# Kernel tuning notes

Measured on AMD Instinct MI355X. Metric: run time of the kernel, lower is better.

The kernel has to match this reference:

```python
import jax, jax.numpy as jnp
import numpy as np

S, N, H, E, V, K = 128, 256, 1024, 512, 32000, 1024  # seq, batch, hidden, embed, vocab, energy channels


def setup_inputs() -> dict:
    key = jax.random.key(0)
    ks = jax.random.split(key, 10)
    s = 0.02
    return {
        "input": jax.random.randint(ks[0], (N,), 0, V),
        "encoder_states": jax.random.normal(ks[1], (S, N, H), jnp.float32),
        "hidden": jax.random.normal(ks[2], (1, N, H), jnp.float32),
        "cell": jax.random.normal(ks[3], (1, N, H), jnp.float32),
        "emb": jax.random.normal(ks[4], (V, E), jnp.float32) * s,
        "W_energy": jax.random.normal(ks[5], (K, 2 * H), jnp.float32) * s,
        "b_energy": jnp.zeros((K,), jnp.float32),
        "W_ih": jax.random.normal(ks[6], (4 * H, H + E), jnp.float32) * s,
        "b_ih": jnp.zeros((4 * H,), jnp.float32),
        "W_hh": jax.random.normal(ks[7], (4 * H, H), jnp.float32) * s,
        "b_hh": jnp.zeros((4 * H,), jnp.float32),
        "W_fc": jax.random.normal(ks[8], (V, H), jnp.float32) * s,
        "b_fc": jnp.zeros((V,), jnp.float32),
    }


def reference(input, encoder_states, hidden, cell, emb, W_energy, b_energy,
              W_ih, b_ih, W_hh, b_hh, W_fc, b_fc):
    seq = encoder_states.shape[0]
    n = encoder_states.shape[1]
    h0 = hidden[0]                                   # [N,H]
    c0 = cell[0]                                     # [N,H]
    emb_x = emb[input]                               # [N,E]

    # additive-attention energy: cat(hidden repeated over S, encoder_states) -> Linear -> ReLU
    h_rep = jnp.broadcast_to(hidden, (seq, n, hidden.shape[2]))
    cat = jnp.concatenate([h_rep, encoder_states], axis=2)          # [S,N,2H]
    energy = jax.nn.relu(jnp.einsum('snh,kh->snk', cat, W_energy) + b_energy)  # [S,N,K]
    # softmax over dim 0 (sequence), independently per (n,k) channel
    attn_last = jax.nn.softmax(energy[..., -1], axis=0)             # [S,N]
    # einsum('snk,snl->knl')[-1] only uses channel k=K-1; contract just that slice
    ctx = jnp.einsum('sn,snl->nl', attn_last, encoder_states)       # [N,H]

    # single-step LSTM (PyTorch gate order i,f,g,o)
    rnn_in = jnp.concatenate([ctx, emb_x], axis=1)                  # [N,H+E]
    gates = rnn_in @ W_ih.T + b_ih + h0 @ W_hh.T + b_hh             # [N,4H]
    i, f, g, o = jnp.split(gates, 4, axis=1)
    c1 = jax.nn.sigmoid(f) * c0 + jax.nn.sigmoid(i) * jnp.tanh(g)
    h1 = jax.nn.sigmoid(o) * jnp.tanh(c1)

    predictions = h1 @ W_fc.T + b_fc                                # [N,V]
    return predictions, h1[None], c1[None]
```

## Files before the change

kernel.cpp:

```cpp
#include <hip/hip_runtime.h>

#define S_DIM 128
#define N_DIM 256
#define H_DIM 1024
#define E_DIM 512
#define V_DIM 32000
#define KE_DIM 1024
#define CIN 2560
#define G4 4096

typedef unsigned short u16;
typedef __bf16 bf16x8 __attribute__((ext_vector_type(8)));
typedef float  f32x4  __attribute__((ext_vector_type(4)));

union U16x8 { uint4 u; bf16x8 b; };

__device__ __forceinline__ unsigned f2bf(float x) {
  unsigned u = __float_as_uint(x);
  return (u + 0x7FFFu + ((u >> 16) & 1u)) >> 16;
}
__device__ __forceinline__ unsigned pk2(float a, float b) {
  return f2bf(a) | (f2bf(b) << 16);
}

__device__ __forceinline__ bf16x8 frag_from_global(const u16* p) {
  U16x8 t; t.u = *(const uint4*)p; return t.b;
}
__device__ __forceinline__ bf16x8 frag_from_lds(const u16* base, int byteoff) {
  U16x8 t; t.u = *(const uint4*)((const char*)base + byteoff); return t.b;
}

__device__ __forceinline__ int loff64(int row, int k) {
  return row * 128 + ((((k >> 3) ^ (row & 7)) << 4) | ((k & 7) << 1));
}
__device__ __forceinline__ int loff128(int row, int k) {
  return row * 256 + ((((k >> 3) ^ (row & 7)) << 4) | ((k & 7) << 1));
}

__device__ __forceinline__ f32x4 mfma16(bf16x8 a, bf16x8 b, f32x4 c) {
  return __builtin_amdgcn_mfma_f32_16x16x32_bf16(a, b, c, 0, 0, 0);
}

__global__ __launch_bounds__(256) void k1_attn(
    const float* __restrict__ enc, const float* __restrict__ hid,
    const float* __restrict__ Wen, const float* __restrict__ ben,
    const int* __restrict__ inp, const float* __restrict__ emb,
    u16* __restrict__ A2)
{
  __shared__ float s_acc[4][H_DIM];
  __shared__ float s_ml[8];
  const int n = blockIdx.x;
  const int t = threadIdx.x;
  const int wave = t >> 6, lane = t & 63;

  const float* Wrow = Wen + (KE_DIM - 1) * (2 * H_DIM);
  float4 we[4];
  #pragma unroll
  for (int ks = 0; ks < 4; ++ks)
    we[ks] = *(const float4*)(Wrow + H_DIM + ks * 256 + lane * 4);

  float hd = 0.f;
  #pragma unroll
  for (int ks = 0; ks < 4; ++ks) {
    float4 wh = *(const float4*)(Wrow + ks * 256 + lane * 4);
    float4 hv = *(const float4*)(hid + n * H_DIM + ks * 256 + lane * 4);
    hd += wh.x * hv.x + wh.y * hv.y + wh.z * hv.z + wh.w * hv.w;
  }
  #pragma unroll
  for (int off = 32; off > 0; off >>= 1) hd += __shfl_xor(hd, off, 64);
  const float ebase = hd + ben[KE_DIM - 1];

  float m = -INFINITY, l = 0.f;
  float4 acc[4];
  #pragma unroll
  for (int ks = 0; ks < 4; ++ks) acc[ks] = make_float4(0.f, 0.f, 0.f, 0.f);

  const long rstride = 4L * N_DIM * H_DIM;
  const float* p = enc + ((long)wave * N_DIM + n) * H_DIM + lane * 4;
  float4 cur[4];
  #pragma unroll
  for (int ks = 0; ks < 4; ++ks) cur[ks] = *(const float4*)(p + ks * 256);

  for (int s = wave; s < S_DIM; s += 4) {
    float4 nxt[4];
    const float* pn = p + rstride;
    const bool has = (s + 4 < S_DIM);
    if (has) {
      #pragma unroll
      for (int ks = 0; ks < 4; ++ks) nxt[ks] = *(const float4*)(pn + ks * 256);
    }
    float d = 0.f;
    #pragma unroll
    for (int ks = 0; ks < 4; ++ks)
      d += we[ks].x * cur[ks].x + we[ks].y * cur[ks].y +
           we[ks].z * cur[ks].z + we[ks].w * cur[ks].w;
    #pragma unroll
    for (int off = 32; off > 0; off >>= 1) d += __shfl_xor(d, off, 64);
    const float e  = fmaxf(ebase + d, 0.f);
    const float nm = fmaxf(m, e);
    const float sc = __expf(m - nm);
    const float pe = __expf(e - nm);
    l = l * sc + pe;
    #pragma unroll
    for (int ks = 0; ks < 4; ++ks) {
      acc[ks].x = acc[ks].x * sc + pe * cur[ks].x;
      acc[ks].y = acc[ks].y * sc + pe * cur[ks].y;
      acc[ks].z = acc[ks].z * sc + pe * cur[ks].z;
      acc[ks].w = acc[ks].w * sc + pe * cur[ks].w;
    }
    m = nm;
    if (has) {
      #pragma unroll
      for (int ks = 0; ks < 4; ++ks) cur[ks] = nxt[ks];
    }
    p = pn;
  }

  #pragma unroll
  for (int ks = 0; ks < 4; ++ks)
    *(float4*)&s_acc[wave][ks * 256 + lane * 4] = acc[ks];
  if (lane == 0) { s_ml[wave] = m; s_ml[4 + wave] = l; }
  __syncthreads();

  const float M = fmaxf(fmaxf(s_ml[0], s_ml[1]), fmaxf(s_ml[2], s_ml[3]));
  const float f0 = __expf(s_ml[0] - M), f1 = __expf(s_ml[1] - M);
  const float f2 = __expf(s_ml[2] - M), f3 = __expf(s_ml[3] - M);
  const float L = s_ml[4] * f0 + s_ml[5] * f1 + s_ml[6] * f2 + s_ml[7] * f3;
  const float invL = 1.0f / L;
  {
    const int e0 = t * 4;
    float v0 = (s_acc[0][e0+0]*f0 + s_acc[1][e0+0]*f1 + s_acc[2][e0+0]*f2 + s_acc[3][e0+0]*f3) * invL;
    float v1 = (s_acc[0][e0+1]*f0 + s_acc[1][e0+1]*f1 + s_acc[2][e0+1]*f2 + s_acc[3][e0+1]*f3) * invL;
    float v2 = (s_acc[0][e0+2]*f0 + s_acc[1][e0+2]*f1 + s_acc[2][e0+2]*f2 + s_acc[3][e0+2]*f3) * invL;
    float v3 = (s_acc[0][e0+3]*f0 + s_acc[1][e0+3]*f1 + s_acc[2][e0+3]*f2 + s_acc[3][e0+3]*f3) * invL;
    uint2 pk; pk.x = pk2(v0, v1); pk.y = pk2(v2, v3);
    *(uint2*)&A2[(long)n * CIN + e0] = pk;
  }

  const int idx = inp[n];
  for (int j = t; j < E_DIM + H_DIM; j += 256) {
    float v = (j < E_DIM) ? emb[(long)idx * E_DIM + j]
                          : hid[n * H_DIM + (j - E_DIM)];
    A2[(long)n * CIN + H_DIM + j] = (u16)f2bf(v);
  }
}

__global__ __launch_bounds__(256) void k2_gates(
    const u16* __restrict__ A2, const float* __restrict__ Wih,
    const float* __restrict__ bih, const float* __restrict__ Whh,
    const float* __restrict__ bhh, float* __restrict__ gates)
{
  __shared__ u16 Blds[16 * 128];
  const int t = threadIdx.x;
  const int wave = t >> 6, lane = t & 63;
  const int quad = lane >> 4, l15 = lane & 15;
  const int j0 = blockIdx.x * 16;
  const int br = t >> 4;
  const int bk = (t & 15) * 8;

  f32x4 acc[4];
  #pragma unroll
  for (int mt = 0; mt < 4; ++mt) acc[mt] = (f32x4){0.f, 0.f, 0.f, 0.f};

  const float* s0 = Wih + (long)(j0 + br) * 1536 + bk;
  float4 v0 = *(const float4*)s0;
  float4 v1 = *(const float4*)(s0 + 4);

  for (int kt = 0; kt < 20; ++kt) {
    const int k0 = kt * 128;
    uint4 pk;
    pk.x = pk2(v0.x, v0.y); pk.y = pk2(v0.z, v0.w);
    pk.z = pk2(v1.x, v1.y); pk.w = pk2(v1.z, v1.w);
    *(uint4*)((char*)Blds + loff128(br, bk)) = pk;
    if (kt + 1 < 20) {
      const int kn = k0 + 128 + bk;
      const float* sn = (kn < 1536) ? (Wih + (long)(j0 + br) * 1536 + kn)
                                    : (Whh + (long)(j0 + br) * 1024 + (kn - 1536));
      v0 = *(const float4*)sn;
      v1 = *(const float4*)(sn + 4);
    }
    __syncthreads();
    #pragma unroll
    for (int kstep = 0; kstep < 4; ++kstep) {
      const int kl = kstep * 32 + quad * 8;
      const bf16x8 bfrag = frag_from_lds(Blds, loff128(l15, kl));
      #pragma unroll
      for (int mt = 0; mt < 4; ++mt) {
        const int row = wave * 64 + mt * 16 + l15;
        const bf16x8 afrag = frag_from_global(A2 + (long)row * CIN + k0 + kl);
        acc[mt] = mfma16(afrag, bfrag, acc[mt]);
      }
    }
    __syncthreads();
  }

  const float bias = bih[j0 + l15] + bhh[j0 + l15];
  #pragma unroll
  for (int mt = 0; mt < 4; ++mt) {
    #pragma unroll
    for (int r = 0; r < 4; ++r) {
      const int row = wave * 64 + mt * 16 + quad * 4 + r;
      gates[(long)row * G4 + j0 + l15] = acc[mt][r] + bias;
    }
  }
}

__global__ __launch_bounds__(256) void k2b_lstm(
    const float* __restrict__ gates, const float* __restrict__ cell,
    float* __restrict__ h1, float* __restrict__ c1, u16* __restrict__ h1b)
{
  const int i = blockIdx.x * 256 + threadIdx.x;
  const int n = i >> 10, h = i & 1023;
  const float* g = gates + (long)n * G4 + h;
  const float gi = g[0], gf = g[1024], gg = g[2048], go = g[3072];
  const float si = 1.f / (1.f + __expf(-gi));
  const float sf = 1.f / (1.f + __expf(-gf));
  const float so = 1.f / (1.f + __expf(-go));
  const float tg = tanhf(gg);
  const float cv = sf * cell[i] + si * tg;
  const float hv = so * tanhf(cv);
  c1[i] = cv;
  h1[i] = hv;
  h1b[i] = (u16)f2bf(hv);
}

__global__ __launch_bounds__(256) void k3_fc(
    const u16* __restrict__ h1b, const float* __restrict__ Wfc,
    const float* __restrict__ bfc, float* __restrict__ out)
{
  __shared__ u16 Blds[64 * 64];
  const int t = threadIdx.x;
  const int wave = t >> 6, lane = t & 63;
  const int quad = lane >> 4, l15 = lane & 15;
  const int j0 = blockIdx.x * 64;
  const int br = t >> 2;
  const int bk = (t & 3) * 16;
  const float* bsrc = Wfc + (long)(j0 + br) * 1024 + bk;

  f32x4 acc[4][4];
  #pragma unroll
  for (int mt = 0; mt < 4; ++mt)
    #pragma unroll
    for (int nt = 0; nt < 4; ++nt) acc[mt][nt] = (f32x4){0.f, 0.f, 0.f, 0.f};

  float4 v0 = *(const float4*)(bsrc);
  float4 v1 = *(const float4*)(bsrc + 4);
  float4 v2 = *(const float4*)(bsrc + 8);
  float4 v3 = *(const float4*)(bsrc + 12);

  for (int kt = 0; kt < 16; ++kt) {
    const int k0 = kt * 64;
    uint4 pa, pb;
    pa.x = pk2(v0.x, v0.y); pa.y = pk2(v0.z, v0.w);
    pa.z = pk2(v1.x, v1.y); pa.w = pk2(v1.z, v1.w);
    pb.x = pk2(v2.x, v2.y); pb.y = pk2(v2.z, v2.w);
    pb.z = pk2(v3.x, v3.y); pb.w = pk2(v3.z, v3.w);
    *(uint4*)((char*)Blds + loff64(br, bk)) = pa;
    *(uint4*)((char*)Blds + loff64(br, bk + 8)) = pb;
    if (kt + 1 < 16) {
      const float* sn = bsrc + (k0 + 64);
      v0 = *(const float4*)(sn);
      v1 = *(const float4*)(sn + 4);
      v2 = *(const float4*)(sn + 8);
      v3 = *(const float4*)(sn + 12);
    }
    __syncthreads();
    #pragma unroll
    for (int kstep = 0; kstep < 2; ++kstep) {
      const int kl = kstep * 32 + quad * 8;
      bf16x8 bfrag[4], afrag[4];
      #pragma unroll
      for (int nt = 0; nt < 4; ++nt)
        bfrag[nt] = frag_from_lds(Blds, loff64(nt * 16 + l15, kl));
      #pragma unroll
      for (int mt = 0; mt < 4; ++mt)
        afrag[mt] = frag_from_global(h1b + (long)(wave * 64 + mt * 16 + l15) * 1024 + k0 + kl);
      #pragma unroll
      for (int mt = 0; mt < 4; ++mt)
        #pragma unroll
        for (int nt = 0; nt < 4; ++nt)
          acc[mt][nt] = mfma16(afrag[mt], bfrag[nt], acc[mt][nt]);
    }
    __syncthreads();
  }

  #pragma unroll
  for (int nt = 0; nt < 4; ++nt) {
    const float bv = bfc[j0 + nt * 16 + l15];
    #pragma unroll
    for (int mt = 0; mt < 4; ++mt) {
      #pragma unroll
      for (int r = 0; r < 4; ++r) {
        const int row = wave * 64 + mt * 16 + quad * 4 + r;
        out[(long)row * V_DIM + j0 + nt * 16 + l15] = acc[mt][nt][r] + bv;
      }
    }
  }
}

extern "C" void kernel_launch(void* const* d_in, const int* in_sizes, int n_in,
                              void* d_out, int out_size, void* d_ws, size_t ws_size,
                              hipStream_t stream) {
  const int*   inp  = (const int*)  d_in[0];
  const float* enc  = (const float*)d_in[1];
  const float* hid  = (const float*)d_in[2];
  const float* cell = (const float*)d_in[3];
  const float* emb  = (const float*)d_in[4];
  const float* Wen  = (const float*)d_in[5];
  const float* ben  = (const float*)d_in[6];
  const float* Wih  = (const float*)d_in[7];
  const float* bih  = (const float*)d_in[8];
  const float* Whh  = (const float*)d_in[9];
  const float* bhh  = (const float*)d_in[10];
  const float* Wfc  = (const float*)d_in[11];
  const float* bfc  = (const float*)d_in[12];

  float* out  = (float*)d_out;
  float* pred = out;
  float* h1   = out + (long)N_DIM * V_DIM;
  float* c1   = h1 + (long)N_DIM * H_DIM;

  char* ws = (char*)d_ws;
  u16*   A2    = (u16*)ws;
  float* gates = (float*)(ws + 1310720);
  u16*   h1b   = (u16*)(ws + 1310720 + 4194304);

  k1_attn <<<N_DIM,            256, 0, stream>>>(enc, hid, Wen, ben, inp, emb, A2);
  k2_gates<<<G4 / 16,          256, 0, stream>>>(A2, Wih, bih, Whh, bhh, gates);
  k2b_lstm<<<(N_DIM*H_DIM)/256,256, 0, stream>>>(gates, cell, h1, c1, h1b);
  k3_fc   <<<V_DIM / 64,       256, 0, stream>>>(h1b, Wfc, bfc, pred);
}
```

Baseline: 425.8 us.

## Fuse attention, LSTM gates and FC into one cooperative persistent kernel

Replaces the four kernel launches with a single cooperative kernel of 256 blocks of 512 threads, using grid.sync between the attention, gate and FC phases. The gate GEMM is reorganised so each block computes the i/f/g/o columns for 4 hidden units and applies the LSTM cell in place, which removes the fp32 gates buffer and the separate elementwise kernel. The FC phase becomes a persistent loop over vocabulary tiles with smaller per-wave tiles. The intent is to remove launch gaps and gate-buffer traffic. The cost is only 256 blocks for the FC GEMM, so fewer waves are resident to hide memory latency, plus the overhead of the grid barriers.

```diff
diff --git a/kernel.cpp b/kernel.cpp
--- a/kernel.cpp
+++ b/kernel.cpp
@@ -1,4 +1,7 @@
 #include <hip/hip_runtime.h>
+#include <hip/hip_cooperative_groups.h>
+
+namespace cg = cooperative_groups;
 
 #define S_DIM 128
 #define N_DIM 256
@@ -7,7 +10,6 @@
 #define V_DIM 32000
 #define KE_DIM 1024
 #define CIN 2560
-#define G4 4096
 
 typedef unsigned short u16;
 typedef __bf16 bf16x8 __attribute__((ext_vector_type(8)));
@@ -41,258 +43,249 @@
   return __builtin_amdgcn_mfma_f32_16x16x32_bf16(a, b, c, 0, 0, 0);
 }
 
-__global__ __launch_bounds__(256) void k1_attn(
-    const float* __restrict__ enc, const float* __restrict__ hid,
-    const float* __restrict__ Wen, const float* __restrict__ ben,
-    const int* __restrict__ inp, const float* __restrict__ emb,
-    u16* __restrict__ A2)
+struct ShP1 { float acc[8][H_DIM]; float ml[16]; };
+struct ShP2 { u16 b[16 * 128]; float sg[256][17]; };
+struct ShP3 { u16 b[64 * 64]; };
+union ShAll { ShP1 p1; ShP2 p2; ShP3 p3; };
+
+__global__ __launch_bounds__(512) void kmega(
+    const int*   __restrict__ inp,  const float* __restrict__ enc,
+    const float* __restrict__ hid,  const float* __restrict__ cell0,
+    const float* __restrict__ emb,  const float* __restrict__ Wen,
+    const float* __restrict__ ben,  const float* __restrict__ Wih,
+    const float* __restrict__ bih,  const float* __restrict__ Whh,
+    const float* __restrict__ bhh,  const float* __restrict__ Wfc,
+    const float* __restrict__ bfc,
+    u16* __restrict__ A2, u16* __restrict__ h1b,
+    float* __restrict__ pred, float* __restrict__ h1, float* __restrict__ c1)
 {
-  __shared__ float s_acc[4][H_DIM];
-  __shared__ float s_ml[8];
-  const int n = blockIdx.x;
-  const int t = threadIdx.x;
-  const int wave = t >> 6, lane = t & 63;
-
-  const float* Wrow = Wen + (KE_DIM - 1) * (2 * H_DIM);
-  float4 we[4];
-  #pragma unroll
-  for (int ks = 0; ks < 4; ++ks)
-    we[ks] = *(const float4*)(Wrow + H_DIM + ks * 256 + lane * 4);
-
-  float hd = 0.f;
-  #pragma unroll
-  for (int ks = 0; ks < 4; ++ks) {
-    float4 wh = *(const float4*)(Wrow + ks * 256 + lane * 4);
-    float4 hv = *(const float4*)(hid + n * H_DIM + ks * 256 + lane * 4);
-    hd += wh.x * hv.x + wh.y * hv.y + wh.z * hv.z + wh.w * hv.w;
-  }
-  #pragma unroll
-  for (int off = 32; off > 0; off >>= 1) hd += __shfl_xor(hd, off, 64);
-  const float ebase = hd + ben[KE_DIM - 1];
-
-  float m = -INFINITY, l = 0.f;
-  float4 acc[4];
-  #pragma unroll
-  for (int ks = 0; ks < 4; ++ks) acc[ks] = make_float4(0.f, 0.f, 0.f, 0.f);
-
-  const long rstride = 4L * N_DIM * H_DIM;
-  const float* p = enc + ((long)wave * N_DIM + n) * H_DIM + lane * 4;
-  float4 cur[4];
-  #pragma unroll
-  for (int ks = 0; ks < 4; ++ks) cur[ks] = *(const float4*)(p + ks * 256);
-
-  for (int s = wave; s < S_DIM; s += 4) {
-    float4 nxt[4];
-    const float* pn = p + rstride;
-    const bool has = (s + 4 < S_DIM);
-    if (has) {
-      #pragma unroll
-      for (int ks = 0; ks < 4; ++ks) nxt[ks] = *(const float4*)(pn + ks * 256);
-    }
-    float d = 0.f;
-    #pragma unroll
-    for (int ks = 0; ks < 4; ++ks)
-      d += we[ks].x * cur[ks].x + we[ks].y * cur[ks].y +
-           we[ks].z * cur[ks].z + we[ks].w * cur[ks].w;
-    #pragma unroll
-    for (int off = 32; off > 0; off >>= 1) d += __shfl_xor(d, off, 64);
-    const float e  = fmaxf(ebase + d, 0.f);
-    const float nm = fmaxf(m, e);
-    const float sc = __expf(m - nm);
-    const float pe = __expf(e - nm);
-    l = l * sc + pe;
-    #pragma unroll
-    for (int ks = 0; ks < 4; ++ks) {
-      acc[ks].x = acc[ks].x * sc + pe * cur[ks].x;
-      acc[ks].y = acc[ks].y * sc + pe * cur[ks].y;
-      acc[ks].z = acc[ks].z * sc + pe * cur[ks].z;
-      acc[ks].w = acc[ks].w * sc + pe * cur[ks].w;
-    }
-    m = nm;
-    if (has) {
-      #pragma unroll
-      for (int ks = 0; ks < 4; ++ks) cur[ks] = nxt[ks];
-    }
-    p = pn;
-  }
-
-  #pragma unroll
-  for (int ks = 0; ks < 4; ++ks)
-    *(float4*)&s_acc[wave][ks * 256 + lane * 4] = acc[ks];
-  if (lane == 0) { s_ml[wave] = m; s_ml[4 + wave] = l; }
-  __syncthreads();
-
-  const float M = fmaxf(fmaxf(s_ml[0], s_ml[1]), fmaxf(s_ml[2], s_ml[3]));
-  const float f0 = __expf(s_ml[0] - M), f1 = __expf(s_ml[1] - M);
-  const float f2 = __expf(s_ml[2] - M), f3 = __expf(s_ml[3] - M);
-  const float L = s_ml[4] * f0 + s_ml[5] * f1 + s_ml[6] * f2 + s_ml[7] * f3;
-  const float invL = 1.0f / L;
-  {
-    const int e0 = t * 4;
-    float v0 = (s_acc[0][e0+0]*f0 + s_acc[1][e0+0]*f1 + s_acc[2][e0+0]*f2 + s_acc[3][e0+0]*f3) * invL;
-    float v1 = (s_acc[0][e0+1]*f0 + s_acc[1][e0+1]*f1 + s_acc[2][e0+1]*f2 + s_acc[3][e0+1]*f3) * invL;
-    float v2 = (s_acc[0][e0+2]*f0 + s_acc[1][e0+2]*f1 + s_acc[2][e0+2]*f2 + s_acc[3][e0+2]*f3) * invL;
-    float v3 = (s_acc[0][e0+3]*f0 + s_acc[1][e0+3]*f1 + s_acc[2][e0+3]*f2 + s_acc[3][e0+3]*f3) * invL;
-    uint2 pk; pk.x = pk2(v0, v1); pk.y = pk2(v2, v3);
-    *(uint2*)&A2[(long)n * CIN + e0] = pk;
-  }
-
-  const int idx = inp[n];
-  for (int j = t; j < E_DIM + H_DIM; j += 256) {
-    float v = (j < E_DIM) ? emb[(long)idx * E_DIM + j]
-                          : hid[n * H_DIM + (j - E_DIM)];
-    A2[(long)n * CIN + H_DIM + j] = (u16)f2bf(v);
-  }
-}
-
-__global__ __launch_bounds__(256) void k2_gates(
-    const u16* __restrict__ A2, const float* __restrict__ Wih,
-    const float* __restrict__ bih, const float* __restrict__ Whh,
-    const float* __restrict__ bhh, float* __restrict__ gates)
-{
-  __shared__ u16 Blds[16 * 128];
-  const int t = threadIdx.x;
+  __shared__ ShAll sh;
+  cg::grid_group grid = cg::this_grid();
+  const int t    = threadIdx.x;
   const int wave = t >> 6, lane = t & 63;
   const int quad = lane >> 4, l15 = lane & 15;
-  const int j0 = blockIdx.x * 16;
-  const int br = t >> 4;
-  const int bk = (t & 15) * 8;
-
-  f32x4 acc[4];
-  #pragma unroll
-  for (int mt = 0; mt < 4; ++mt) acc[mt] = (f32x4){0.f, 0.f, 0.f, 0.f};
-
-  const float* s0 = Wih + (long)(j0 + br) * 1536 + bk;
-  float4 v0 = *(const float4*)s0;
-  float4 v1 = *(const float4*)(s0 + 4);
-
-  for (int kt = 0; kt < 20; ++kt) {
-    const int k0 = kt * 128;
-    uint4 pk;
-    pk.x = pk2(v0.x, v0.y); pk.y = pk2(v0.z, v0.w);
-    pk.z = pk2(v1.x, v1.y); pk.w = pk2(v1.z, v1.w);
-    *(uint4*)((char*)Blds + loff128(br, bk)) = pk;
-    if (kt + 1 < 20) {
-      const int kn = k0 + 128 + bk;
-      const float* sn = (kn < 1536) ? (Wih + (long)(j0 + br) * 1536 + kn)
-                                    : (Whh + (long)(j0 + br) * 1024 + (kn - 1536));
-      v0 = *(const float4*)sn;
-      v1 = *(const float4*)(sn + 4);
-    }
+
+  {
+    const int n = blockIdx.x;
+    const float* Wrow = Wen + (KE_DIM - 1) * (2 * H_DIM);
+    float4 we[4];
+    #pragma unroll
+    for (int ks = 0; ks < 4; ++ks)
+      we[ks] = *(const float4*)(Wrow + H_DIM + ks * 256 + lane * 4);
+
+    float hd = 0.f;
+    #pragma unroll
+    for (int ks = 0; ks < 4; ++ks) {
+      float4 wh = *(const float4*)(Wrow + ks * 256 + lane * 4);
+      float4 hv = *(const float4*)(hid + n * H_DIM + ks * 256 + lane * 4);
+      hd += wh.x * hv.x + wh.y * hv.y + wh.z * hv.z + wh.w * hv.w;
+    }
+    #pragma unroll
+    for (int off = 32; off > 0; off >>= 1) hd += __shfl_xor(hd, off, 64);
+    const float ebase = hd + ben[KE_DIM - 1];
+
+    float m = -INFINITY, l = 0.f;
+    float4 acc[4];
+    #pragma unroll
+    for (int ks = 0; ks < 4; ++ks) acc[ks] = make_float4(0.f, 0.f, 0.f, 0.f);
+
+    const long rstride = 8L * N_DIM * H_DIM;
+    const float* p = enc + ((long)wave * N_DIM + n) * H_DIM + lane * 4;
+    float4 cur[4];
+    #pragma unroll
+    for (int ks = 0; ks < 4; ++ks) cur[ks] = *(const float4*)(p + ks * 256);
+
+    for (int s = wave; s < S_DIM; s += 8) {
+      float4 nxt[4];
+      const float* pn = p + rstride;
+      const bool has = (s + 8 < S_DIM);
+      if (has) {
+        #pragma unroll
+        for (int ks = 0; ks < 4; ++ks) nxt[ks] = *(const float4*)(pn + ks * 256);
+      }
+      float d = 0.f;
+      #pragma unroll
+      for (int ks = 0; ks < 4; ++ks)
+        d += we[ks].x * cur[ks].x + we[ks].y * cur[ks].y +
+             we[ks].z * cur[ks].z + we[ks].w * cur[ks].w;
+      #pragma unroll
+      for (int off = 32; off > 0; off >>= 1) d += __shfl_xor(d, off, 64);
+      const float e  = fmaxf(ebase + d, 0.f);
+      const float nm = fmaxf(m, e);
+      const float sc = __expf(m - nm);
+      const float pe = __expf(e - nm);
+      l = l * sc + pe;
+      #pragma unroll
+      for (int ks = 0; ks < 4; ++ks) {
+        acc[ks].x = acc[ks].x * sc + pe * cur[ks].x;
+        acc[ks].y = acc[ks].y * sc + pe * cur[ks].y;
+        acc[ks].z = acc[ks].z * sc + pe * cur[ks].z;
+        acc[ks].w = acc[ks].w * sc + pe * cur[ks].w;
+      }
+      m = nm;
+      if (has) {
+        #pragma unroll
+        for (int ks = 0; ks < 4; ++ks) cur[ks] = nxt[ks];
+      }
+      p = pn;
+    }
+
+    #pragma unroll
+    for (int ks = 0; ks < 4; ++ks)
+      *(float4*)&sh.p1.acc[wave][ks * 256 + lane * 4] = acc[ks];
+    if (lane == 0) { sh.p1.ml[wave] = m; sh.p1.ml[8 + wave] = l; }
     __syncthreads();
-    #pragma unroll
-    for (int kstep = 0; kstep < 4; ++kstep) {
-      const int kl = kstep * 32 + quad * 8;
-      const bf16x8 bfrag = frag_from_lds(Blds, loff128(l15, kl));
-      #pragma unroll
-      for (int mt = 0; mt < 4; ++mt) {
-        const int row = wave * 64 + mt * 16 + l15;
-        const bf16x8 afrag = frag_from_global(A2 + (long)row * CIN + k0 + kl);
-        acc[mt] = mfma16(afrag, bfrag, acc[mt]);
-      }
+
+    float M = sh.p1.ml[0];
+    #pragma unroll
+    for (int w = 1; w < 8; ++w) M = fmaxf(M, sh.p1.ml[w]);
+    float f[8]; float L = 0.f;
+    #pragma unroll
+    for (int w = 0; w < 8; ++w) { f[w] = __expf(sh.p1.ml[w] - M); L += sh.p1.ml[8 + w] * f[w]; }
+    const float invL = 1.0f / L;
+    {
+      const int e0 = t * 2;
+      float v0 = 0.f, v1 = 0.f;
+      #pragma unroll
+      for (int w = 0; w < 8; ++w) {
+        v0 += sh.p1.acc[w][e0]     * f[w];
+        v1 += sh.p1.acc[w][e0 + 1] * f[w];
+      }
+      *(unsigned*)&A2[(long)n * CIN + e0] = pk2(v0 * invL, v1 * invL);
+    }
+    const int idx = inp[n];
+    for (int j = t; j < E_DIM + H_DIM; j += 512) {
+      float v = (j < E_DIM) ? emb[(long)idx * E_DIM + j]
+                            : hid[n * H_DIM + (j - E_DIM)];
+      A2[(long)n * CIN + H_DIM + j] = (u16)f2bf(v);
+    }
+  }
+  __threadfence();
+  grid.sync();
+
+  {
+    const int b  = blockIdx.x;
+    const int br = t >> 5;
+    const int bk = (t & 31) * 4;
+    const int jbr = (br >> 2) * H_DIM + b * 4 + (br & 3);
+
+    f32x4 acc[2];
+    acc[0] = (f32x4){0.f, 0.f, 0.f, 0.f};
+    acc[1] = (f32x4){0.f, 0.f, 0.f, 0.f};
+
+    float4 v = *(const float4*)(Wih + (long)jbr * 1536 + bk);
+
+    for (int kt = 0; kt < 20; ++kt) {
+      const int k0 = kt * 128;
+      uint2 pk; pk.x = pk2(v.x, v.y); pk.y = pk2(v.z, v.w);
+      *(uint2*)((char*)sh.p2.b + loff128(br, bk)) = pk;
+      if (kt + 1 < 20) {
+        const int kn = k0 + 128 + bk;
+        const float* sn = (kn < 1536) ? (Wih + (long)jbr * 1536 + kn)
+                                      : (Whh + (long)jbr * H_DIM + (kn - 1536));
+        v = *(const float4*)sn;
+      }
+      __syncthreads();
+      #pragma unroll
+      for (int kstep = 0; kstep < 4; ++kstep) {
+        const int kl = kstep * 32 + quad * 8;
+        const bf16x8 bfrag = frag_from_lds(sh.p2.b, loff128(l15, kl));
+        #pragma unroll
+        for (int mt = 0; mt < 2; ++mt) {
+          const int row = wave * 32 + mt * 16 + l15;
+          const bf16x8 afrag = frag_from_global(A2 + (long)row * CIN + k0 + kl);
+          acc[mt] = mfma16(afrag, bfrag, acc[mt]);
+        }
+      }
+      __syncthreads();
+    }
+
+    {
+      const int jj = (l15 >> 2) * H_DIM + b * 4 + (l15 & 3);
+      const float bias = bih[jj] + bhh[jj];
+      #pragma unroll
+      for (int mt = 0; mt < 2; ++mt)
+        #pragma unroll
+        for (int r = 0; r < 4; ++r)
+          sh.p2.sg[wave * 32 + mt * 16 + quad * 4 + r][l15] = acc[mt][r] + bias;
     }
     __syncthreads();
+    #pragma unroll
+    for (int u = 0; u < 2; ++u) {
+      const int id = t + u * 512;
+      const int n = id >> 2, q = id & 3, h = b * 4 + q;
+      const float gi = sh.p2.sg[n][q],      gf = sh.p2.sg[n][4 + q];
+      const float gg = sh.p2.sg[n][8 + q],  go = sh.p2.sg[n][12 + q];
+      const float si = 1.f / (1.f + __expf(-gi));
+      const float sf = 1.f / (1.f + __expf(-gf));
+      const float so = 1.f / (1.f + __expf(-go));
+      const float tg = tanhf(gg);
+      const float cv = sf * cell0[(long)n * H_DIM + h] + si * tg;
+      const float hv = so * tanhf(cv);
+      c1 [(long)n * H_DIM + h] = cv;
+      h1 [(long)n * H_DIM + h] = hv;
+      h1b[(long)n * H_DIM + h] = (u16)f2bf(hv);
+    }
   }
-
-  const float bias = bih[j0 + l15] + bhh[j0 + l15];
-  #pragma unroll
-  for (int mt = 0; mt < 4; ++mt) {
-    #pragma unroll
-    for (int r = 0; r < 4; ++r) {
-      const int row = wave * 64 + mt * 16 + quad * 4 + r;
-      gates[(long)row * G4 + j0 + l15] = acc[mt][r] + bias;
-    }
-  }
-}
-
-__global__ __launch_bounds__(256) void k2b_lstm(
-    const float* __restrict__ gates, const float* __restrict__ cell,
-    float* __restrict__ h1, float* __restrict__ c1, u16* __restrict__ h1b)
-{
-  const int i = blockIdx.x * 256 + threadIdx.x;
-  const int n = i >> 10, h = i & 1023;
-  const float* g = gates + (long)n * G4 + h;
-  const float gi = g[0], gf = g[1024], gg = g[2048], go = g[3072];
-  const float si = 1.f / (1.f + __expf(-gi));
-  const float sf = 1.f / (1.f + __expf(-gf));
-  const float so = 1.f / (1.f + __expf(-go));
-  const float tg = tanhf(gg);
-  const float cv = sf * cell[i] + si * tg;
-  const float hv = so * tanhf(cv);
-  c1[i] = cv;
-  h1[i] = hv;
-  h1b[i] = (u16)f2bf(hv);
-}
-
-__global__ __launch_bounds__(256) void k3_fc(
-    const u16* __restrict__ h1b, const float* __restrict__ Wfc,
-    const float* __restrict__ bfc, float* __restrict__ out)
-{
-  __shared__ u16 Blds[64 * 64];
-  const int t = threadIdx.x;
-  const int wave = t >> 6, lane = t & 63;
-  const int quad = lane >> 4, l15 = lane & 15;
-  const int j0 = blockIdx.x * 64;
-  const int br = t >> 2;
-  const int bk = (t & 3) * 16;
-  const float* bsrc = Wfc + (long)(j0 + br) * 1024 + bk;
-
-  f32x4 acc[4][4];
-  #pragma unroll
-  for (int mt = 0; mt < 4; ++mt)
-    #pragma unroll
-    for (int nt = 0; nt < 4; ++nt) acc[mt][nt] = (f32x4){0.f, 0.f, 0.f, 0.f};
-
-  float4 v0 = *(const float4*)(bsrc);
-  float4 v1 = *(const float4*)(bsrc + 4);
-  float4 v2 = *(const float4*)(bsrc + 8);
-  float4 v3 = *(const float4*)(bsrc + 12);
-
-  for (int kt = 0; kt < 16; ++kt) {
-    const int k0 = kt * 64;
-    uint4 pa, pb;
-    pa.x = pk2(v0.x, v0.y); pa.y = pk2(v0.z, v0.w);
-    pa.z = pk2(v1.x, v1.y); pa.w = pk2(v1.z, v1.w);
-    pb.x = pk2(v2.x, v2.y); pb.y = pk2(v2.z, v2.w);
-    pb.z = pk2(v3.x, v3.y); pb.w = pk2(v3.z, v3.w);
-    *(uint4*)((char*)Blds + loff64(br, bk)) = pa;
-    *(uint4*)((char*)Blds + loff64(br, bk + 8)) = pb;
-    if (kt + 1 < 16) {
-      const float* sn = bsrc + (k0 + 64);
-      v0 = *(const float4*)(sn);
-      v1 = *(const float4*)(sn + 4);
-      v2 = *(const float4*)(sn + 8);
-      v3 = *(const float4*)(sn + 12);
-    }
-    __syncthreads();
-    #pragma unroll
-    for (int kstep = 0; kstep < 2; ++kstep) {
-      const int kl = kstep * 32 + quad * 8;
-      bf16x8 bfrag[4], afrag[4];
-      #pragma unroll
-      for (int nt = 0; nt < 4; ++nt)
-        bfrag[nt] = frag_from_lds(Blds, loff64(nt * 16 + l15, kl));
-      #pragma unroll
-      for (int mt = 0; mt < 4; ++mt)
-        afrag[mt] = frag_from_global(h1b + (long)(wave * 64 + mt * 16 + l15) * 1024 + k0 + kl);
-      #pragma unroll
-      for (int mt = 0; mt < 4; ++mt)
+  __threadfence();
+  grid.sync();
+
+  for (int tile = blockIdx.x; tile < V_DIM / 64; tile += 256) {
+    const int j0 = tile * 64;
+    const int br = t >> 3;
+    const int bk = (t & 7) * 8;
+    const float* bsrc = Wfc + (long)(j0 + br) * H_DIM + bk;
+
+    f32x4 acc[2][4];
+    #pragma unroll
+    for (int mt = 0; mt < 2; ++mt)
+      #pragma unroll
+      for (int nt = 0; nt < 4; ++nt) acc[mt][nt] = (f32x4){0.f, 0.f, 0.f, 0.f};
+
+    float4 v0 = *(const float4*)(bsrc);
+    float4 v1 = *(const float4*)(bsrc + 4);
+
+    for (int kt = 0; kt < 16; ++kt) {
+      const int k0 = kt * 64;
+      uint4 pa;
+      pa.x = pk2(v0.x, v0.y); pa.y = pk2(v0.z, v0.w);
+      pa.z = pk2(v1.x, v1.y); pa.w = pk2(v1.z, v1.w);
+      *(uint4*)((char*)sh.p3.b + loff64(br, bk)) = pa;
+      if (kt + 1 < 16) {
+        const float* sn = bsrc + (k0 + 64);
+        v0 = *(const float4*)(sn);
+        v1 = *(const float4*)(sn + 4);
+      }
+      __syncthreads();
+      #pragma unroll
+      for (int kstep = 0; kstep < 2; ++kstep) {
+        const int kl = kstep * 32 + quad * 8;
+        bf16x8 bfrag[4], afrag[2];
         #pragma unroll
         for (int nt = 0; nt < 4; ++nt)
-          acc[mt][nt] = mfma16(afrag[mt], bfrag[nt], acc[mt][nt]);
-    }
-    __syncthreads();
-  }
-
-  #pragma unroll
-  for (int nt = 0; nt < 4; ++nt) {
-    const float bv = bfc[j0 + nt * 16 + l15];
-    #pragma unroll
-    for (int mt = 0; mt < 4; ++mt) {
-      #pragma unroll
-      for (int r = 0; r < 4; ++r) {
-        const int row = wave * 64 + mt * 16 + quad * 4 + r;
-        out[(long)row * V_DIM + j0 + nt * 16 + l15] = acc[mt][nt][r] + bv;
+          bfrag[nt] = frag_from_lds(sh.p3.b, loff64(nt * 16 + l15, kl));
+        #pragma unroll
+        for (int mt = 0; mt < 2; ++mt)
+          afrag[mt] = frag_from_global(h1b + (long)(wave * 32 + mt * 16 + l15) * H_DIM + k0 + kl);
+        #pragma unroll
+        for (int mt = 0; mt < 2; ++mt)
+          #pragma unroll
+          for (int nt = 0; nt < 4; ++nt)
+            acc[mt][nt] = mfma16(afrag[mt], bfrag[nt], acc[mt][nt]);
+      }
+      __syncthreads();
+    }
+
+    #pragma unroll
+    for (int nt = 0; nt < 4; ++nt) {
+      const float bv = bfc[j0 + nt * 16 + l15];
+      #pragma unroll
+      for (int mt = 0; mt < 2; ++mt) {
+        #pragma unroll
+        for (int r = 0; r < 4; ++r) {
+          const int row = wave * 32 + mt * 16 + quad * 4 + r;
+          pred[(long)row * V_DIM + j0 + nt * 16 + l15] = acc[mt][nt][r] + bv;
+        }
       }
     }
   }
@@ -304,7 +297,7 @@
   const int*   inp  = (const int*)  d_in[0];
   const float* enc  = (const float*)d_in[1];
   const float* hid  = (const float*)d_in[2];
-  const float* cell = (const float*)d_in[3];
+  const float* cel  = (const float*)d_in[3];
   const float* emb  = (const float*)d_in[4];
   const float* Wen  = (const float*)d_in[5];
   const float* ben  = (const float*)d_in[6];
@@ -321,12 +314,14 @@
   float* c1   = h1 + (long)N_DIM * H_DIM;
 
   char* ws = (char*)d_ws;
-  u16*   A2    = (u16*)ws;
-  float* gates = (float*)(ws + 1310720);
-  u16*   h1b   = (u16*)(ws + 1310720 + 4194304);
-
-  k1_attn <<<N_DIM,            256, 0, stream>>>(enc, hid, Wen, ben, inp, emb, A2);
-  k2_gates<<<G4 / 16,          256, 0, stream>>>(A2, Wih, bih, Whh, bhh, gates);
-  k2b_lstm<<<(N_DIM*H_DIM)/256,256, 0, stream>>>(gates, cell, h1, c1, h1b);
-  k3_fc   <<<V_DIM / 64,       256, 0, stream>>>(h1b, Wfc, bfc, pred);
-}
+  u16* A2  = (u16*)ws;
+  u16* h1b = (u16*)(ws + 1310720);
+
+  void* args[] = {
+    (void*)&inp, (void*)&enc, (void*)&hid, (void*)&cel, (void*)&emb,
+    (void*)&Wen, (void*)&ben, (void*)&Wih, (void*)&bih, (void*)&Whh,
+    (void*)&bhh, (void*)&Wfc, (void*)&bfc,
+    (void*)&A2, (void*)&h1b, (void*)&pred, (void*)&h1, (void*)&c1
+  };
+  hipLaunchCooperativeKernel((void*)kmega, dim3(N_DIM), dim3(512), args, 0, stream);
+}
```

After: 593.8 us. 39.5% more time.
